# Performance work log

Measured on AMD Instinct MI355X. Metric: run time of the kernel, lower is better.

Reference implementation:

```python
import jax, jax.numpy as jnp
import numpy as np
from jax.scipy.special import logsumexp

B, N_LC, N_TE, D = 4, 2048, 2048, 256
ITERS = 100  # Sinkhorn iterations


def _mlp2(x, W1, b1, W2, b2):
    # 2-layer MLP with ReLU (DETR-style MLP, num_layers=2)
    h = jax.nn.relu(x @ W1.T + b1)
    return h @ W2.T + b2


def _log_optimal_transport(scores, alpha, iters):
    b, m, n = scores.shape
    ms = jnp.float32(m)
    ns = jnp.float32(n)
    # augment score matrix with dustbin row/col -> [b, m+1, n+1]
    bins0 = jnp.broadcast_to(alpha, (b, m, 1))
    bins1 = jnp.broadcast_to(alpha, (b, 1, n))
    binsc = jnp.broadcast_to(alpha, (b, 1, 1))
    Z = jnp.concatenate([
        jnp.concatenate([scores, bins0], axis=-1),
        jnp.concatenate([bins1, binsc], axis=-1)], axis=1)
    norm = -jnp.log(ms + ns)
    log_mu = jnp.concatenate([jnp.full((m,), norm), jnp.log(ns)[None] + norm])
    log_nu = jnp.concatenate([jnp.full((n,), norm), jnp.log(ms)[None] + norm])
    log_mu = jnp.broadcast_to(log_mu[None], (b, m + 1))
    log_nu = jnp.broadcast_to(log_nu[None], (b, n + 1))

    def step(carry, _):
        u, v = carry
        u = log_mu - logsumexp(Z + v[:, None, :], axis=2)
        v = log_nu - logsumexp(Z + u[:, :, None], axis=1)
        return (u, v), None

    u0 = jnp.zeros_like(log_mu)
    v0 = jnp.zeros_like(log_nu)
    (u, v), _ = jax.lax.scan(step, (u0, v0), None, length=iters)
    return Z + u[:, :, None] + v[:, None, :] - norm


def setup_inputs() -> dict:
    key = jax.random.key(0)
    ks = jax.random.split(key, 8)
    s = 1.0 / np.sqrt(D).astype(np.float32)
    return {
        "quer_feat_lc": jax.random.normal(ks[0], (B, N_LC, D), jnp.float32),
        "quer_feat_te": jax.random.normal(ks[1], (B, N_TE, D), jnp.float32),
        "W1_lc": jax.random.normal(ks[2], (D, D), jnp.float32) * s,
        "b1_lc": jnp.zeros((D,), jnp.float32),
        "W2_lc": jax.random.normal(ks[3], (D, D), jnp.float32) * s,
        "b2_lc": jnp.zeros((D,), jnp.float32),
        "W1_te": jax.random.normal(ks[4], (D, D), jnp.float32) * s,
        "b1_te": jnp.zeros((D,), jnp.float32),
        "W2_te": jax.random.normal(ks[5], (D, D), jnp.float32) * s,
        "b2_te": jnp.zeros((D,), jnp.float32),
        "bin_score": jnp.ones((), jnp.float32),
    }


def reference(quer_feat_lc, quer_feat_te, W1_lc, b1_lc, W2_lc, b2_lc,
              W1_te, b1_te, W2_te, b2_te, bin_score):
    f1 = _mlp2(quer_feat_lc, W1_lc, b1_lc, W2_lc, b2_lc)  # [B, N_LC, D]
    f2 = _mlp2(quer_feat_te, W1_te, b1_te, W2_te, b2_te)  # [B, N_TE, D]
    scores = jnp.einsum('bnc,bmc->bnm', f1, f2) / jnp.sqrt(jnp.float32(D))
    Z = _log_optimal_transport(scores, bin_score, ITERS)  # [B, N_LC+1, N_TE+1]
    return jnp.exp(Z)
```

## Files before the change

kernel.cpp:

```cpp
#include <hip/hip_runtime.h>
#include <hip/hip_fp16.h>

#define NQ   2048
#define NB   4
#define DD   256
#define M1   2049
#define STR  2064
#define UVS  1088
#define SINK_ITERS 100
#define PNWG 256
#define PTPB 1024

typedef __attribute__((ext_vector_type(8))) short short8;
typedef __attribute__((ext_vector_type(4))) float floatx4;
typedef _Float16 h2 __attribute__((ext_vector_type(2)));

__device__ __forceinline__ unsigned short f2bf(float f) {
  unsigned u = __float_as_uint(f);
  u += 0x7FFF + ((u >> 16) & 1);
  return (unsigned short)(u >> 16);
}

__device__ __forceinline__ unsigned char f2fp8(float f) {
  unsigned short u = __half_as_ushort(__float2half(f));
  return (unsigned char)((u + 0x7F + ((u >> 8) & 1)) >> 8);
}

__device__ __forceinline__ h2 as_h2(unsigned x) {
  union { unsigned u; h2 h; } c; c.u = x; return c.h;
}

__global__ void k_prep(const float* __restrict__ x_lc, const float* __restrict__ x_te,
                       const float* __restrict__ w1lc, const float* __restrict__ w2lc,
                       const float* __restrict__ w1te, const float* __restrict__ w2te,
                       unsigned short* __restrict__ Xlc, unsigned short* __restrict__ Xte,
                       unsigned short* __restrict__ Wb, __half* __restrict__ E,
                       const float* __restrict__ alphaPtr, unsigned* __restrict__ ev,
                       unsigned* __restrict__ bar) {
  const int NX4 = (NB * NQ * DD) / 4;
  const int NW4 = (DD * DD) / 4;
  const int bx = blockIdx.x;
  if (bx < 4352) {
    int i4 = bx * 256 + threadIdx.x;
    const float* src; unsigned short* dst; int off;
    if (i4 < NX4)            { src = x_lc; dst = Xlc; off = i4; }
    else if (i4 < 2 * NX4)   { src = x_te; dst = Xte; off = i4 - NX4; }
    else {
      int k = i4 - 2 * NX4;
      int seg = k / NW4;
      off = k - seg * NW4;
      src = (seg == 0) ? w1lc : (seg == 1) ? w2lc : (seg == 2) ? w1te : w2te;
      dst = Wb + seg * 65536;
    }
    float4 f = ((const float4*)src)[off];
    ushort4 o;
    o.x = f2bf(f.x); o.y = f2bf(f.y); o.z = f2bf(f.z); o.w = f2bf(f.w);
    ((ushort4*)dst)[off] = o;
    return;
  }
  const int idx = (bx - 4352) * 256 + threadIdx.x;
  const float ea = __expf(*alphaPtr);
  const int n1 = NB * NQ * 16;
  if (idx < n1) {
    int b = idx / (NQ * 16);
    int rr = idx - b * NQ * 16;
    int i = rr >> 4;
    int j = 2048 + (rr & 15);
    E[((long)b * M1 + i) * STR + j] = (j == 2048) ? __float2half(ea) : __float2half(0.f);
    return;
  }
  int k = idx - n1;
  if (k < NB * STR) {
    int b = k / STR;
    int j = k - b * STR;
    E[((long)b * M1 + 2048) * STR + j] = (j <= 2048) ? __float2half(ea) : __float2half(0.f);
    return;
  }
  int m = k - NB * STR;
  if (m < NB * UVS) {
    int bloc = m / UVS;
    int slot = m - bloc * UVS;
    ev[m] = (slot < 1024) ? 0x6C006C00u
          : (slot == 1024 ? __float_as_uint(4096.f) : 0u);
    return;
  }
  int q = m - NB * UVS;
  if (q < 2048) bar[q] = 0u;
}

template<int MODE>
__global__ __launch_bounds__(256, 2)
void k_gemm_bt(const unsigned short* __restrict__ A,
               const unsigned short* __restrict__ Bt,
               void* __restrict__ Out, void* __restrict__ Out8, void* __restrict__ OutT8,
               const float* __restrict__ bias, const float* __restrict__ bias2,
               int K, long aBatch, long bBatch, long oBatch, int ostride)
{
  __shared__ __align__(16) unsigned short lA[128 * 32];
  __shared__ __align__(16) unsigned short lB[128 * 32];
  const int tid  = threadIdx.x;
  const int lane = tid & 63;
  const int w    = tid >> 6;
  const int wm   = (w >> 1) * 64;
  const int wn   = (w & 1) * 64;
  const long bz  = blockIdx.z;
  const unsigned short* Ab = A  + bz * aBatch + (long)blockIdx.y * 128 * K;
  const unsigned short* Bb = Bt + bz * bBatch + (long)blockIdx.x * 128 * K;
  const float* bp = (bz == 0) ? bias : bias2;

  floatx4 acc[4][4];
  #pragma unroll
  for (int i = 0; i < 4; i++)
    #pragma unroll
    for (int j = 0; j < 4; j++) acc[i][j] = (floatx4){0.f, 0.f, 0.f, 0.f};

  for (int kt = 0; kt < K; kt += 32) {
    __syncthreads();
    #pragma unroll
    for (int s0 = 0; s0 < 512; s0 += 256) {
      int s = s0 + tid;
      int row = s >> 2, part = s & 3;
      ((uint4*)lA)[s] = *(const uint4*)(Ab + (long)row * K + kt + part * 8);
      ((uint4*)lB)[s] = *(const uint4*)(Bb + (long)row * K + kt + part * 8);
    }
    __syncthreads();
    const int kq = (lane >> 4) * 8;
    const int rl = lane & 15;
    short8 af[4], bf[4];
    #pragma unroll
    for (int t = 0; t < 4; t++) {
      af[t] = *(const short8*)(lA + (wm + t * 16 + rl) * 32 + kq);
      bf[t] = *(const short8*)(lB + (wn + t * 16 + rl) * 32 + kq);
    }
    #pragma unroll
    for (int i = 0; i < 4; i++)
      #pragma unroll
      for (int j = 0; j < 4; j++)
        acc[i][j] = __builtin_amdgcn_mfma_f32_16x16x32_bf16(af[i], bf[j], acc[i][j], 0, 0, 0);
  }

  const int cl = lane & 15, qd = lane >> 4;
  #pragma unroll
  for (int i = 0; i < 4; i++)
    #pragma unroll
    for (int j = 0; j < 4; j++) {
      const int col = blockIdx.x * 128 + wn + j * 16 + cl;
      const float bcol = (MODE >= 2) ? 0.f : bp[col];
      const long rowbase = (long)blockIdx.y * 128 + wm + i * 16 + qd * 4;
      unsigned pk = 0;
      #pragma unroll
      for (int r = 0; r < 4; r++) {
        const long row = rowbase + r;
        float v = acc[i][j][r];
        if (MODE == 0) {
          v += bcol; v = v > 0.f ? v : 0.f;
          ((unsigned short*)Out)[bz * oBatch + row * ostride + col] = f2bf(v);
        } else if (MODE == 1) {
          v += bcol;
          ((unsigned short*)Out)[bz * oBatch + row * ostride + col] = f2bf(v);
        } else {
          v *= 0.0625f;
          v = fminf(fmaxf(v, -15.f), 10.9f);
          float e = __expf(v);
          const long idx = bz * oBatch + row * ostride + col;
          ((__half*)Out)[idx] = __float2half(e);
          unsigned char f8 = f2fp8(e);
          ((unsigned char*)Out8)[idx] = f8;
          pk |= (unsigned)f8 << (8 * r);
        }
      }
      if (MODE == 2) {
        *(unsigned*)((unsigned char*)OutT8 + bz * oBatch + (long)col * ostride + rowbase) = pk;
      }
    }
}

__device__ __forceinline__ void st_u32_agent(unsigned* p, unsigned v) {
  __hip_atomic_store(p, v, __ATOMIC_RELAXED, __HIP_MEMORY_SCOPE_AGENT);
}
__device__ __forceinline__ unsigned ld_u32_agent(const unsigned* p) {
  return __hip_atomic_load(p, __ATOMIC_RELAXED, __HIP_MEMORY_SCOPE_AGENT);
}

__device__ __forceinline__ float wave_sum(float s) {
  #pragma unroll
  for (int o = 32; o; o >>= 1) s += __shfl_xor(s, o);
  return s;
}

__device__ __forceinline__ float dot16e5(uint4 hv, const unsigned* wp, float s) {
  const unsigned* u = (const unsigned*)&hv;
#if __has_builtin(__builtin_amdgcn_fdot2) && __has_builtin(__builtin_amdgcn_perm)
  #pragma unroll
  for (int q = 0; q < 4; q++) {
    unsigned lo = __builtin_amdgcn_perm(u[q], 0u, 0x05000400u);
    unsigned hi = __builtin_amdgcn_perm(u[q], 0u, 0x07000600u);
    s = __builtin_amdgcn_fdot2(as_h2(lo), as_h2(wp[2 * q]),     s, false);
    s = __builtin_amdgcn_fdot2(as_h2(hi), as_h2(wp[2 * q + 1]), s, false);
  }
#else
  const unsigned char* p = (const unsigned char*)&hv;
  #pragma unroll
  for (int t = 0; t < 16; t++) {
    unsigned short he = (unsigned short)p[t] << 8;
    unsigned wdw = wp[t >> 1];
    unsigned short hw = (t & 1) ? (unsigned short)(wdw >> 16) : (unsigned short)(wdw & 0xFFFF);
    s += __half2float(*reinterpret_cast<__half*>(&he)) *
         __half2float(*reinterpret_cast<__half*>(&hw));
  }
#endif
  return s;
}

__global__ __launch_bounds__(PTPB, 4)
void k_sink(const unsigned char* __restrict__ E8, const unsigned char* __restrict__ ET8,
            unsigned* __restrict__ eu, unsigned* __restrict__ ev,
            const float* __restrict__ alphaPtr, unsigned* __restrict__ bar)
{
  __shared__ __align__(16) unsigned char rows[131072];
  __shared__ __align__(16) unsigned svh[1160];
  __shared__ float sdust;
  const int tid  = threadIdx.x;
  const int wg   = blockIdx.x;
  const int b    = wg >> 6;
  const int g    = wg & 63;
  const int wv   = tid >> 6;
  const int lane = tid & 63;
  const int r0   = (g * 16 + wv) * 2;
  const float ea = __expf(alphaPtr[0]);
  const unsigned char* E8r  = E8  + ((long)b * M1 + r0) * STR;
  const unsigned char* ET8r = ET8 + ((long)b * M1 + r0) * STR;
  unsigned* ub = eu + b * UVS;
  unsigned* vb = ev + b * UVS;
  unsigned* cnt = bar + b * 64;
  unsigned* gen = bar + b * 64 + 32;
  const bool dustwave = (g == 63) && (wv == 15);
  const int sslot = (tid >> 9) * 576 + (tid & 511) + ((tid & 511) >> 3);

  {
    uint4* dw = (uint4*)(rows + wv * 8192);
    dw[lane]       = *(const uint4*)(E8r  +        lane * 16);
    dw[64 + lane]  = *(const uint4*)(E8r  + 1024 + lane * 16);
    dw[128 + lane] = *(const uint4*)(E8r  + STR  +        lane * 16);
    dw[192 + lane] = *(const uint4*)(E8r  + STR  + 1024 + lane * 16);
    dw[256 + lane] = *(const uint4*)(ET8r +        lane * 16);
    dw[320 + lane] = *(const uint4*)(ET8r + 1024 + lane * 16);
    dw[384 + lane] = *(const uint4*)(ET8r + STR  +        lane * 16);
    dw[448 + lane] = *(const uint4*)(ET8r + STR  + 1024 + lane * 16);
  }

  const unsigned* w0 = svh + 9 * lane;
  const unsigned* w1 = svh + 576 + 9 * lane;
  const unsigned ONES2 = 0x3C003C00u;

  unsigned phase = 0;
  for (int it = 0; it < 2 * SINK_ITERS; ++it) {
    const unsigned* vin = (it & 1) ? ub : vb;
    unsigned*      vout = (it & 1) ? vb : ub;

    {
      unsigned pkv = ld_u32_agent(vin + tid);
      svh[sslot] = pkv;
      if (tid == 0) sdust = __uint_as_float(ld_u32_agent(vin + 1024));
    }
    __syncthreads();

    const unsigned char* Rl = rows + wv * 8192 + ((it & 1) << 12);
    uint4 h0c0 = *(const uint4*)(Rl +        lane * 16);
    uint4 h0c1 = *(const uint4*)(Rl + 1024 + lane * 16);
    uint4 h1c0 = *(const uint4*)(Rl + 2048 + lane * 16);
    uint4 h1c1 = *(const uint4*)(Rl + 3072 + lane * 16);
    float a0 = dot16e5(h0c1, w1, dot16e5(h0c0, w0, 0.f));
    float a1 = dot16e5(h1c1, w1, dot16e5(h1c0, w0, 0.f));
    a0 = wave_sum(a0);
    a1 = wave_sum(a1);
    if (lane == 0) {
      const float wd = ea * sdust;
      float u0 = 4096.f / (a0 + wd);
      float u1 = 4096.f / (a1 + wd);
      unsigned pk = ((unsigned)__half_as_ushort(__float2half(u1)) << 16)
                  |  (unsigned)__half_as_ushort(__float2half(u0));
      st_u32_agent(vout + (r0 >> 1), pk);
    }

    if (dustwave) {
      float s = 0.f;
#if __has_builtin(__builtin_amdgcn_fdot2)
      #pragma unroll
      for (int k = 0; k < 8; k++) s = __builtin_amdgcn_fdot2(as_h2(w0[k]), as_h2(ONES2), s, false);
      #pragma unroll
      for (int k = 0; k < 8; k++) s = __builtin_amdgcn_fdot2(as_h2(w1[k]), as_h2(ONES2), s, false);
#else
      #pragma unroll
      for (int k = 0; k < 8; k++) {
        unsigned a = w0[k], c = w1[k];
        unsigned short x0 = (unsigned short)a, x1 = (unsigned short)(a >> 16);
        unsigned short y0 = (unsigned short)c, y1 = (unsigned short)(c >> 16);
        s += __half2float(*reinterpret_cast<__half*>(&x0)) + __half2float(*reinterpret_cast<__half*>(&x1))
           + __half2float(*reinterpret_cast<__half*>(&y0)) + __half2float(*reinterpret_cast<__half*>(&y1));
      }
#endif
      s = wave_sum(s);
      if (lane == 0)
        st_u32_agent(vout + 1024, __float_as_uint(8388608.f / (ea * (s + sdust))));
    }

    ++phase;
    __syncthreads();
    if (tid == 0) {
      unsigned gpre = ld_u32_agent(gen);
      unsigned old = __hip_atomic_fetch_add(cnt, 1u, __ATOMIC_RELAXED, __HIP_MEMORY_SCOPE_AGENT);
      if (old == phase * 64u - 1u) {
        __hip_atomic_store(gen, phase, __ATOMIC_RELAXED, __HIP_MEMORY_SCOPE_AGENT);
      } else {
        while (gpre < phase) {
          __builtin_amdgcn_s_sleep(1);
          gpre = ld_u32_agent(gen);
        }
      }
    }
    __syncthreads();
  }
}

__global__ void k_final(const __half* __restrict__ E, const unsigned* __restrict__ eu,
                        const unsigned* __restrict__ ev, float* __restrict__ out) {
  const int wvb = blockIdx.x;
  const int b = wvb / M1;
  const int i = wvb - b * M1;
  const __half* R = E + ((long)b * M1 + i) * STR;
  const unsigned* ub = eu + b * UVS;
  const unsigned* vb = ev + b * UVS;
  float ui;
  if (i < 2048) {
    unsigned d = ub[i >> 1];
    unsigned short h = (i & 1) ? (unsigned short)(d >> 16) : (unsigned short)(d & 0xFFFF);
    ui = __half2float(*reinterpret_cast<const __half*>(&h));
  } else {
    ui = __uint_as_float(ub[1024]);
  }
  ui *= (1.f / 4096.f);
  float* orow = out + ((long)b * M1 + i) * M1;
  for (int j = threadIdx.x; j < M1; j += blockDim.x) {
    float vj;
    if (j < 2048) {
      unsigned d = vb[j >> 1];
      unsigned short h = (j & 1) ? (unsigned short)(d >> 16) : (unsigned short)(d & 0xFFFF);
      vj = __half2float(*reinterpret_cast<const __half*>(&h));
    } else {
      vj = __uint_as_float(vb[1024]);
    }
    orow[j] = __half2float(R[j]) * ui * vj;
  }
}

extern "C" void kernel_launch(void* const* d_in, const int* in_sizes, int n_in,
                              void* d_out, int out_size, void* d_ws, size_t ws_size,
                              hipStream_t stream) {
  const float* x_lc  = (const float*)d_in[0];
  const float* x_te  = (const float*)d_in[1];
  const float* W1_lc = (const float*)d_in[2];
  const float* b1_lc = (const float*)d_in[3];
  const float* W2_lc = (const float*)d_in[4];
  const float* b2_lc = (const float*)d_in[5];
  const float* W1_te = (const float*)d_in[6];
  const float* b1_te = (const float*)d_in[7];
  const float* W2_te = (const float*)d_in[8];
  const float* b2_te = (const float*)d_in[9];
  const float* alpha = (const float*)d_in[10];

  char* ws = (char*)d_ws;
  unsigned short* Xlc = (unsigned short*)(ws + 0);
  unsigned short* Wb  = (unsigned short*)(ws + 8388608);
  unsigned short* H   = (unsigned short*)(ws + 8912896);
  unsigned short* F   = (unsigned short*)(ws + 0);
  __half* E  = (__half*)(ws + 21495808);
  unsigned char* E8  = (unsigned char*)(ws + 55328896);
  unsigned char* ET8 = (unsigned char*)(ws + 72245440);
  unsigned* eu  = (unsigned*)(ws + 89161984);
  unsigned* ev  = (unsigned*)(ws + 89195008);
  unsigned* bar = (unsigned*)(ws + 89228032);

  unsigned short* Xte = Xlc + 2097152;

  k_prep<<<4352 + 570, 256, 0, stream>>>(x_lc, x_te, W1_lc, W2_lc, W1_te, W2_te,
                                         Xlc, Xte, Wb, E, alpha, ev, bar);

  k_gemm_bt<0><<<dim3(2, 64, 2), 256, 0, stream>>>(Xlc, Wb,         H, nullptr, nullptr,
                                                   b1_lc, b1_te, DD, 2097152, 131072, 2097152, DD);
  k_gemm_bt<1><<<dim3(2, 64, 2), 256, 0, stream>>>(H,   Wb + 65536, F, nullptr, nullptr,
                                                   b2_lc, b2_te, DD, 2097152, 131072, 2097152, DD);

  unsigned short* F1 = F;
  unsigned short* F2 = F + 2097152;
  const long ab = (long)NQ * DD;
  const long ob = (long)M1 * STR;
  k_gemm_bt<2><<<dim3(16, 16, NB), 256, 0, stream>>>(F1, F2, E, E8, ET8,
                                                     nullptr, nullptr, DD, ab, ab, ob, STR);

  k_sink<<<PNWG, PTPB, 0, stream>>>(E8, ET8, eu, ev, alpha, bar);

  k_final<<<NB * M1, 256, 0, stream>>>(E, eu, ev, (float*)d_out);
}
```

Baseline: 799.1 us.

## Restructure Sinkhorn grid barrier, load dual vector into registers, vectorize final kernel

```diff
diff --git a/kernel.cpp b/kernel.cpp
--- a/kernel.cpp
+++ b/kernel.cpp
@@ -181,6 +181,9 @@
 __device__ __forceinline__ unsigned ld_u32_agent(const unsigned* p) {
   return __hip_atomic_load(p, __ATOMIC_RELAXED, __HIP_MEMORY_SCOPE_AGENT);
 }
+__device__ __forceinline__ unsigned long long ld64_agent(const unsigned long long* p) {
+  return __hip_atomic_load(p, __ATOMIC_RELAXED, __HIP_MEMORY_SCOPE_AGENT);
+}
 
 __device__ __forceinline__ float wave_sum(float s) {
   #pragma unroll
@@ -218,8 +221,6 @@
             const float* __restrict__ alphaPtr, unsigned* __restrict__ bar)
 {
   __shared__ __align__(16) unsigned char rows[131072];
-  __shared__ __align__(16) unsigned svh[1160];
-  __shared__ float sdust;
   const int tid  = threadIdx.x;
   const int wg   = blockIdx.x;
   const int b    = wg >> 6;
@@ -235,7 +236,6 @@
   unsigned* cnt = bar + b * 64;
   unsigned* gen = bar + b * 64 + 32;
   const bool dustwave = (g == 63) && (wv == 15);
-  const int sslot = (tid >> 9) * 576 + (tid & 511) + ((tid & 511) >> 3);
 
   {
     uint4* dw = (uint4*)(rows + wv * 8192);
@@ -249,33 +249,43 @@
     dw[448 + lane] = *(const uint4*)(ET8r + STR  + 1024 + lane * 16);
   }
 
-  const unsigned* w0 = svh + 9 * lane;
-  const unsigned* w1 = svh + 576 + 9 * lane;
   const unsigned ONES2 = 0x3C003C00u;
 
-  unsigned phase = 0;
   for (int it = 0; it < 2 * SINK_ITERS; ++it) {
     const unsigned* vin = (it & 1) ? ub : vb;
     unsigned*      vout = (it & 1) ? vb : ub;
 
-    {
-      unsigned pkv = ld_u32_agent(vin + tid);
-      svh[sslot] = pkv;
-      if (tid == 0) sdust = __uint_as_float(ld_u32_agent(vin + 1024));
+    if (tid == 0) {
+      while (ld_u32_agent(gen) < (unsigned)it)
+        __builtin_amdgcn_s_sleep(1);
     }
     __syncthreads();
+
+    const unsigned long long* vq = (const unsigned long long*)vin;
+    unsigned w[16];
+    unsigned long long q;
+    q = ld64_agent(vq + 4 * lane + 0);        w[0]  = (unsigned)q; w[1]  = (unsigned)(q >> 32);
+    q = ld64_agent(vq + 4 * lane + 1);        w[2]  = (unsigned)q; w[3]  = (unsigned)(q >> 32);
+    q = ld64_agent(vq + 4 * lane + 2);        w[4]  = (unsigned)q; w[5]  = (unsigned)(q >> 32);
+    q = ld64_agent(vq + 4 * lane + 3);        w[6]  = (unsigned)q; w[7]  = (unsigned)(q >> 32);
+    q = ld64_agent(vq + 256 + 4 * lane + 0);  w[8]  = (unsigned)q; w[9]  = (unsigned)(q >> 32);
+    q = ld64_agent(vq + 256 + 4 * lane + 1);  w[10] = (unsigned)q; w[11] = (unsigned)(q >> 32);
+    q = ld64_agent(vq + 256 + 4 * lane + 2);  w[12] = (unsigned)q; w[13] = (unsigned)(q >> 32);
+    q = ld64_agent(vq + 256 + 4 * lane + 3);  w[14] = (unsigned)q; w[15] = (unsigned)(q >> 32);
+    float sd = 0.f;
+    if (lane == 0) sd = __uint_as_float(ld_u32_agent(vin + 1024));
 
     const unsigned char* Rl = rows + wv * 8192 + ((it & 1) << 12);
     uint4 h0c0 = *(const uint4*)(Rl +        lane * 16);
     uint4 h0c1 = *(const uint4*)(Rl + 1024 + lane * 16);
     uint4 h1c0 = *(const uint4*)(Rl + 2048 + lane * 16);
     uint4 h1c1 = *(const uint4*)(Rl + 3072 + lane * 16);
-    float a0 = dot16e5(h0c1, w1, dot16e5(h0c0, w0, 0.f));
-    float a1 = dot16e5(h1c1, w1, dot16e5(h1c0, w0, 0.f));
+    float a0 = dot16e5(h0c1, w + 8, dot16e5(h0c0, w + 0, 0.f));
+    float a1 = dot16e5(h1c1, w + 8, dot16e5(h1c0, w + 0, 0.f));
     a0 = wave_sum(a0);
     a1 = wave_sum(a1);
     if (lane == 0) {
-      const float wd = ea * sdust;
+      const float wd = ea * sd;
       float u0 = 4096.f / (a0 + wd);
       float u1 = 4096.f / (a1 + wd);
       unsigned pk = ((unsigned)__half_as_ushort(__float2half(u1)) << 16)
@@ -287,39 +297,27 @@
       float s = 0.f;
 #if __has_builtin(__builtin_amdgcn_fdot2)
       #pragma unroll
-      for (int k = 0; k < 8; k++) s = __builtin_amdgcn_fdot2(as_h2(w0[k]), as_h2(ONES2), s, false);
-      #pragma unroll
-      for (int k = 0; k < 8; k++) s = __builtin_amdgcn_fdot2(as_h2(w1[k]), as_h2(ONES2), s, false);
+      for (int k = 0; k < 16; k++) s = __builtin_amdgcn_fdot2(as_h2(w[k]), as_h2(ONES2), s, false);
 #else
       #pragma unroll
-      for (int k = 0; k < 8; k++) {
-        unsigned a = w0[k], c = w1[k];
+      for (int k = 0; k < 16; k++) {
+        unsigned a = w[k];
         unsigned short x0 = (unsigned short)a, x1 = (unsigned short)(a >> 16);
-        unsigned short y0 = (unsigned short)c, y1 = (unsigned short)(c >> 16);
-        s += __half2float(*reinterpret_cast<__half*>(&x0)) + __half2float(*reinterpret_cast<__half*>(&x1))
-           + __half2float(*reinterpret_cast<__half*>(&y0)) + __half2float(*reinterpret_cast<__half*>(&y1));
+        s += __half2float(*reinterpret_cast<__half*>(&x0))
+           + __half2float(*reinterpret_cast<__half*>(&x1));
       }
 #endif
       s = wave_sum(s);
       if (lane == 0)
-        st_u32_agent(vout + 1024, __float_as_uint(8388608.f / (ea * (s + sdust))));
-    }
-
-    ++phase;
+        st_u32_agent(vout + 1024, __float_as_uint(8388608.f / (ea * (s + sd))));
+    }
+
     __syncthreads();
     if (tid == 0) {
-      unsigned gpre = ld_u32_agent(gen);
       unsigned old = __hip_atomic_fetch_add(cnt, 1u, __ATOMIC_RELAXED, __HIP_MEMORY_SCOPE_AGENT);
-      if (old == phase * 64u - 1u) {
-        __hip_atomic_store(gen, phase, __ATOMIC_RELAXED, __HIP_MEMORY_SCOPE_AGENT);
-      } else {
-        while (gpre < phase) {
-          __builtin_amdgcn_s_sleep(1);
-          gpre = ld_u32_agent(gen);
-        }
-      }
-    }
-    __syncthreads();
+      if (old == (unsigned)(it + 1) * 64u - 1u)
+        __hip_atomic_store(gen, (unsigned)(it + 1), __ATOMIC_RELAXED, __HIP_MEMORY_SCOPE_AGENT);
+    }
   }
 }
 
@@ -340,17 +338,20 @@
     ui = __uint_as_float(ub[1024]);
   }
   ui *= (1.f / 4096.f);
-  float* orow = out + ((long)b * M1 + i) * M1;
-  for (int j = threadIdx.x; j < M1; j += blockDim.x) {
-    float vj;
-    if (j < 2048) {
-      unsigned d = vb[j >> 1];
-      unsigned short h = (j & 1) ? (unsigned short)(d >> 16) : (unsigned short)(d & 0xFFFF);
-      vj = __half2float(*reinterpret_cast<const __half*>(&h));
-    } else {
-      vj = __uint_as_float(vb[1024]);
-    }
-    orow[j] = __half2float(R[j]) * ui * vj;
+  float* orow = out + (long)wvb * M1;
+  for (int t = threadIdx.x; t < 1024; t += blockDim.x) {
+    unsigned vd = vb[t];
+    unsigned ed = *(const unsigned*)(R + 2 * t);
+    const __half2 vh = *reinterpret_cast<const __half2*>(&vd);
+    const __half2 eh = *reinterpret_cast<const __half2*>(&ed);
+    float2 vf = __half22float2(vh);
+    float2 ef = __half22float2(eh);
+    orow[2 * t]     = ef.x * ui * vf.x;
+    orow[2 * t + 1] = ef.y * ui * vf.y;
+  }
+  if (threadIdx.x == 0) {
+    float vd = __uint_as_float(vb[1024]);
+    orow[2048] = __half2float(R[2048]) * ui * vd;
   }
 }
 
```

Measured after the change: 972.4 us. 21.7% more time.
